# Optimization experiments

Measured on AMD Instinct MI355X. Metric: run time of the kernel, lower is better.

## Reference

```python
import jax, jax.numpy as jnp
import numpy as np

DIM = 1024
NUM_HEADS = 16


def setup_inputs() -> dict:
    key = jax.random.key(0)
    ks = jax.random.split(key, 6)
    B, N, C = 2, 2048, DIM
    input_qv = jax.random.normal(ks[0], (B, N, C), dtype=jnp.float32)
    input_k = jax.random.normal(ks[1], (B, N, C), dtype=jnp.float32)
    # Linear weights stored [in, out]; qkv_bias=False so qv/k have no bias.
    s = 1.0 / np.sqrt(C)
    W_qv = jax.random.uniform(ks[2], (C, 2 * C), dtype=jnp.float32, minval=-s, maxval=s)
    W_k = jax.random.uniform(ks[3], (C, C), dtype=jnp.float32, minval=-s, maxval=s)
    W_proj = jax.random.uniform(ks[4], (C, C), dtype=jnp.float32, minval=-s, maxval=s)
    b_proj = jax.random.uniform(ks[5], (C,), dtype=jnp.float32, minval=-s, maxval=s)
    return {"input_qv": input_qv, "input_k": input_k, "W_qv": W_qv,
            "W_k": W_k, "W_proj": W_proj, "b_proj": b_proj}


def reference(input_qv, input_k, W_qv, W_k, W_proj, b_proj):
    B, N, C = input_qv.shape
    H = NUM_HEADS
    Dh = C // H
    scale = Dh ** -0.5
    # qv projection -> [B, N, 2, H, Dh] -> q, v each [B, H, N, Dh]
    qv = (input_qv @ W_qv).reshape(B, N, 2, H, Dh)
    q = jnp.transpose(qv[:, :, 0], (0, 2, 1, 3))  # [B, H, N, Dh]
    v = jnp.transpose(qv[:, :, 1], (0, 2, 1, 3))  # [B, H, N, Dh]
    k = jnp.transpose((input_k @ W_k).reshape(B, N, H, Dh), (0, 2, 1, 3))  # [B, H, N, Dh]
    # explicit QK^T softmax V (dropout ratio 0 -> identity)
    atten = jnp.einsum('bhnd,bhmd->bhnm', q, k) * scale  # [B, H, N, N]
    atten = jax.nn.softmax(atten, axis=-1)
    x = jnp.einsum('bhnm,bhmd->bhnd', atten, v)  # [B, H, N, Dh]
    x = jnp.transpose(x, (0, 2, 1, 3)).reshape(B, N, C)
    return x @ W_proj + b_proj
```

## Files before the change

kernel.cpp:

```cpp
#include <hip/hip_runtime.h>
#include <stdint.h>

#define BATCH 2
#define SEQ   2048
#define DIM   1024
#define NH    16
#define DH    64

typedef short bf16x8 __attribute__((ext_vector_type(8)));
typedef float floatx4 __attribute__((ext_vector_type(4)));

__device__ __forceinline__ int swz(int r) { return (r ^ (r >> 2)) & 3; }

#if __has_builtin(__builtin_amdgcn_exp2f)
#define EXP2(x) __builtin_amdgcn_exp2f(x)
#else
#define EXP2(x) __expf((x) * 0.6931471805599453f)
#endif

__device__ __forceinline__ uint32_t pack_bf16_rne(float x0, float x1) {
    uint32_t u0 = __float_as_uint(x0), u1 = __float_as_uint(x1);
    u0 += 0x7FFFu + ((u0 >> 16) & 1);
    u1 += 0x7FFFu + ((u1 >> 16) & 1);
    return (u0 >> 16) | (u1 & 0xFFFF0000u);
}

__device__ __forceinline__ ushort bf16_rne1(float x) {
    uint32_t u = __float_as_uint(x);
    u += 0x7FFFu + ((u >> 16) & 1);
    return (ushort)(u >> 16);
}

#define KSCALE 0.18033688011112042f

__global__ __launch_bounds__(256, 3)
void gemm_qvk(const float* __restrict__ Aqv, const float* __restrict__ Akp,
              const float* __restrict__ Wqv, const float* __restrict__ Wkp,
              uint32_t* __restrict__ qh, ushort* __restrict__ vt,
              uint32_t* __restrict__ kh)
{
    __shared__ uint32_t Ah[128 * 16], Bh[128 * 16];

    const int t    = threadIdx.x;
    const int lane = t & 63;
    const int w    = t >> 6;
    const int wm   = w & 1, wn = w >> 1;
    const int quad = lane >> 4, l15 = lane & 15;
    const int bx   = blockIdx.x;
    const bool is_qv = (bx < 16);
    const float* Af = is_qv ? Aqv : Akp;
    const float* Bf = is_qv ? Wqv : Wkp;
    const int N    = is_qv ? 2048 : 1024;
    const int n0   = (is_qv ? bx : bx - 16) * 128;
    const int m0   = blockIdx.y * 128;

    const int ar  = t >> 1;
    const int ab0 = (t & 1) * 2;
    const int as  = swz(ar);
    const int bc  = (t & 31) * 4;
    const int bk  = (t >> 5) * 4;
    const int bb  = bk >> 3;
    const int bp  = (bk & 7) >> 1;
    const bool nsel = ((bc >> 4) & 1) != 0;

    floatx4 acc[4][4];
    #pragma unroll
    for (int i = 0; i < 4; i++)
        #pragma unroll
        for (int j = 0; j < 4; j++)
            #pragma unroll
            for (int e = 0; e < 4; e++) acc[i][j][e] = 0.0f;

    float f[16];
    float4 g4[4];
    {
        #pragma unroll
        for (int i = 0; i < 4; i++)
            *(float4*)&f[i * 4] =
                *(const float4*)&Af[(size_t)(m0 + ar) * 1024 + ab0 * 8 + i * 4];
        #pragma unroll
        for (int j = 0; j < 4; j++)
            g4[j] = *(const float4*)&Bf[(size_t)(bk + j) * N + n0 + bc];
    }

    for (int k0 = 0; k0 < 1024; k0 += 32) {
        if (k0) __syncthreads();
        {
            uint32_t hi[8];
            #pragma unroll
            for (int j = 0; j < 8; j++) hi[j] = pack_bf16_rne(f[2 * j], f[2 * j + 1]);
            int i0 = ar * 16 + ((ab0 ^ as) * 4);
            int i1 = ar * 16 + (((ab0 + 1) ^ as) * 4);
            *(uint4*)&Ah[i0] = make_uint4(hi[0], hi[1], hi[2], hi[3]);
            *(uint4*)&Ah[i1] = make_uint4(hi[4], hi[5], hi[6], hi[7]);
        }
        {
            #pragma unroll
            for (int i = 0; i < 4; i++) {
                int n = bc + (i ^ (nsel ? 1 : 0));
                float e0 = nsel ? ((const float*)&g4[0])[i ^ 1] : ((const float*)&g4[0])[i];
                float e1 = nsel ? ((const float*)&g4[1])[i ^ 1] : ((const float*)&g4[1])[i];
                float e2 = nsel ? ((const float*)&g4[2])[i ^ 1] : ((const float*)&g4[2])[i];
                float e3 = nsel ? ((const float*)&g4[3])[i ^ 1] : ((const float*)&g4[3])[i];
                uint32_t u0 = pack_bf16_rne(e0, e1);
                uint32_t u1 = pack_bf16_rne(e2, e3);
                int bi = n * 16 + ((bb ^ swz(n)) * 4) + bp;
                *(uint2*)&Bh[bi] = make_uint2(u0, u1);
            }
        }
        __syncthreads();

        if (k0 + 32 < 1024) {
            #pragma unroll
            for (int i = 0; i < 4; i++)
                *(float4*)&f[i * 4] =
                    *(const float4*)&Af[(size_t)(m0 + ar) * 1024 + (k0 + 32) + ab0 * 8 + i * 4];
            #pragma unroll
            for (int j = 0; j < 4; j++)
                g4[j] = *(const float4*)&Bf[(size_t)(k0 + 32 + bk + j) * N + n0 + bc];
        }

        bf16x8 vb[4];
        #pragma unroll
        for (int fn = 0; fn < 4; fn++) {
            int br = wn * 64 + fn * 16 + l15;
            int bi = br * 16 + ((quad ^ swz(br)) * 4);
            vb[fn] = *(const bf16x8*)&Bh[bi];
        }
        #pragma unroll
        for (int fm = 0; fm < 4; fm++) {
            int arow = wm * 64 + fm * 16 + l15;
            int ai = arow * 16 + ((quad ^ swz(arow)) * 4);
            bf16x8 va = *(const bf16x8*)&Ah[ai];
            #pragma unroll
            for (int fn = 0; fn < 4; fn++)
                acc[fm][fn] = __builtin_amdgcn_mfma_f32_16x16x32_bf16(vb[fn], va, acc[fm][fn], 0, 0, 0);
        }
    }

    #pragma unroll
    for (int fm = 0; fm < 4; fm++) {
        int row = m0 + wm * 64 + fm * 16 + l15;
        #pragma unroll
        for (int fn = 0; fn < 4; fn++) {
            int colb = n0 + wn * 64 + fn * 16 + quad * 4;
            floatx4 a = acc[fm][fn];
            if (is_qv) {
                if (colb < 1024) {
                    uint32_t u0 = pack_bf16_rne(a[0], a[1]);
                    uint32_t u1 = pack_bf16_rne(a[2], a[3]);
                    size_t wi = (size_t)row * 512 + (colb >> 1);
                    *(uint2*)&qh[wi] = make_uint2(u0, u1);
                } else {
                    int hh = (colb - 1024) >> 6;
                    int d0 = (colb - 1024) & 63;
                    #pragma unroll
                    for (int j = 0; j < 4; j++)
                        vt[(size_t)(hh * 64 + d0 + j) * 4096 + row] = bf16_rne1(a[j]);
                }
            } else {
                uint32_t u0 = pack_bf16_rne(a[0] * KSCALE, a[1] * KSCALE);
                uint32_t u1 = pack_bf16_rne(a[2] * KSCALE, a[3] * KSCALE);
                size_t wi = (size_t)row * 512 + (colb >> 1);
                *(uint2*)&kh[wi] = make_uint2(u0, u1);
            }
        }
    }
}

__global__ __launch_bounds__(256, 3)
void gemm_projB(const uint32_t* __restrict__ Ag,
                const float* __restrict__ Bf, const float* __restrict__ bias,
                float* __restrict__ Cf, float* __restrict__ P1)
{
    __shared__ uint32_t Ah[128 * 16], Bh[128 * 16];

    const int t    = threadIdx.x;
    const int lane = t & 63;
    const int w    = t >> 6;
    const int wm   = w & 1, wn = w >> 1;
    const int quad = lane >> 4, l15 = lane & 15;
    const int m0 = blockIdx.y * 128, n0 = blockIdx.x * 128;
    const int kz = blockIdx.z;
    const int k0 = kz * 512;
    const int N  = 1024;

    const int bc  = (t & 31) * 4;
    const int bk  = (t >> 5) * 4;
    const int bb  = bk >> 3;
    const int bp  = (bk & 7) >> 1;
    const bool nsel = ((bc >> 4) & 1) != 0;

    const int arow0 = t >> 2, akbl = t & 3;
    const int arow1 = (t + 256) >> 2;

    floatx4 acc[4][4];
    #pragma unroll
    for (int i = 0; i < 4; i++)
        #pragma unroll
        for (int j = 0; j < 4; j++)
            #pragma unroll
            for (int e = 0; e < 4; e++) acc[i][j][e] = 0.0f;

    uint4 gA0, gA1;
    float4 g4[4];
    {
        size_t s0 = (size_t)(m0 + arow0) * 512 + (k0 >> 1) + akbl * 4;
        size_t s1 = (size_t)(m0 + arow1) * 512 + (k0 >> 1) + akbl * 4;
        gA0 = *(const uint4*)&Ag[s0];
        gA1 = *(const uint4*)&Ag[s1];
        #pragma unroll
        for (int j = 0; j < 4; j++)
            g4[j] = *(const float4*)&Bf[(size_t)(k0 + bk + j) * N + n0 + bc];
    }

    for (int kk = 0; kk < 512; kk += 32) {
        if (kk) __syncthreads();
        {
            int dst0 = arow0 * 16 + ((akbl ^ swz(arow0)) * 4);
            int dst1 = arow1 * 16 + ((akbl ^ swz(arow1)) * 4);
            *(uint4*)&Ah[dst0] = gA0;
            *(uint4*)&Ah[dst1] = gA1;
        }
        {
            #pragma unroll
            for (int i = 0; i < 4; i++) {
                int n = bc + (i ^ (nsel ? 1 : 0));
                float e0 = nsel ? ((const float*)&g4[0])[i ^ 1] : ((const float*)&g4[0])[i];
                float e1 = nsel ? ((const float*)&g4[1])[i ^ 1] : ((const float*)&g4[1])[i];
                float e2 = nsel ? ((const float*)&g4[2])[i ^ 1] : ((const float*)&g4[2])[i];
                float e3 = nsel ? ((const float*)&g4[3])[i ^ 1] : ((const float*)&g4[3])[i];
                uint32_t u0 = pack_bf16_rne(e0, e1);
                uint32_t u1 = pack_bf16_rne(e2, e3);
                int bi = n * 16 + ((bb ^ swz(n)) * 4) + bp;
                *(uint2*)&Bh[bi] = make_uint2(u0, u1);
            }
        }
        __syncthreads();

        if (kk + 32 < 512) {
            const int kg = k0 + kk + 32;
            size_t s0 = (size_t)(m0 + arow0) * 512 + (kg >> 1) + akbl * 4;
            size_t s1 = (size_t)(m0 + arow1) * 512 + (kg >> 1) + akbl * 4;
            gA0 = *(const uint4*)&Ag[s0];
            gA1 = *(const uint4*)&Ag[s1];
            #pragma unroll
            for (int j = 0; j < 4; j++)
                g4[j] = *(const float4*)&Bf[(size_t)(kg + bk + j) * N + n0 + bc];
        }

        bf16x8 vb[4];
        #pragma unroll
        for (int fn = 0; fn < 4; fn++) {
            int br = wn * 64 + fn * 16 + l15;
            int bi = br * 16 + ((quad ^ swz(br)) * 4);
            vb[fn] = *(const bf16x8*)&Bh[bi];
        }
        #pragma unroll
        for (int fm = 0; fm < 4; fm++) {
            int arow = wm * 64 + fm * 16 + l15;
            int ai = arow * 16 + ((quad ^ swz(arow)) * 4);
            bf16x8 va = *(const bf16x8*)&Ah[ai];
            #pragma unroll
            for (int fn = 0; fn < 4; fn++)
                acc[fm][fn] = __builtin_amdgcn_mfma_f32_16x16x32_bf16(vb[fn], va, acc[fm][fn], 0, 0, 0);
        }
    }

    #pragma unroll
    for (int fm = 0; fm < 4; fm++) {
        int row = m0 + wm * 64 + fm * 16 + l15;
        #pragma unroll
        for (int fn = 0; fn < 4; fn++) {
            int colb = n0 + wn * 64 + fn * 16 + quad * 4;
            floatx4 a = acc[fm][fn];
            float4 v;
            if (kz == 0) {
                float4 bb4 = *(const float4*)&bias[colb];
                v.x = a[0] + bb4.x; v.y = a[1] + bb4.y;
                v.z = a[2] + bb4.z; v.w = a[3] + bb4.w;
                *(float4*)&Cf[(size_t)row * N + colb] = v;
            } else {
                v.x = a[0]; v.y = a[1]; v.z = a[2]; v.w = a[3];
                *(float4*)&P1[(size_t)row * N + colb] = v;
            }
        }
    }
}

__global__ __launch_bounds__(256)
void add_partial(const float4* __restrict__ p1, float4* __restrict__ out, int n4)
{
    int i = blockIdx.x * 256 + threadIdx.x;
    int stride = gridDim.x * 256;
    for (; i < n4; i += stride) {
        float4 a = out[i];
        float4 b = p1[i];
        a.x += b.x; a.y += b.y; a.z += b.z; a.w += b.w;
        out[i] = a;
    }
}

#define FST 34
__global__ __launch_bounds__(256, 2)
void flash_attn(const uint32_t* __restrict__ qhg,
                const uint32_t* __restrict__ khg,
                const uint32_t* __restrict__ vtg,
                uint32_t* __restrict__ xhg)
{
    __shared__ uint32_t Kh[64 * FST];
    __shared__ uint32_t Vt[64 * FST];
    __shared__ uint32_t Pt[128 * FST];

    const int t    = threadIdx.x;
    const int lane = t & 63;
    const int w    = t >> 6;
    const int quad = lane >> 4, l15 = lane & 15;
    const int qb = blockIdx.x;
    const int h  = blockIdx.y;
    const int b  = blockIdx.z;

    const size_t rowbase = (size_t)b * SEQ;

    bf16x8 vq[2][2];
    {
        #pragma unroll
        for (int nf = 0; nf < 2; nf++) {
            size_t row = rowbase + qb * 128 + w * 32 + nf * 16 + l15;
            size_t gw = row * 512 + h * 32 + quad * 4;
            #pragma unroll
            for (int s = 0; s < 2; s++)
                vq[s][nf] = *(const bf16x8*)&qhg[gw + s * 16];
        }
    }

    const int krow = t >> 2, kc0 = (t & 3) * 8;
    const int vd = t >> 2, vc = t & 3;
    const size_t vrow = (size_t)(h * 64 + vd) * 2048 + (rowbase >> 1);
    uint4 pk0, pk1, pv0, pv1;
    {
        size_t gw = (rowbase + krow) * 512 + h * 32 + kc0;
        pk0 = *(const uint4*)&khg[gw];
        pk1 = *(const uint4*)&khg[gw + 4];
        size_t vw = vrow + vc * 8;
        pv0 = *(const uint4*)&vtg[vw];
        pv1 = *(const uint4*)&vtg[vw + 4];
    }

    float m_i[2] = {-INFINITY, -INFINITY};
    float l_i[2] = {0.0f, 0.0f};
    floatx4 acc_o[2][4];
    #pragma unroll
    for (int nf = 0; nf < 2; nf++)
        #pragma unroll
        for (int fm = 0; fm < 4; fm++)
            #pragma unroll
            for (int e = 0; e < 4; e++) acc_o[nf][fm][e] = 0.0f;

    for (int kt = 0; kt < SEQ / 64; kt++) {
        __syncthreads();
        *(uint4*)&Kh[krow * FST + kc0]     = pk0;
        *(uint4*)&Kh[krow * FST + kc0 + 4] = pk1;
        {
            int vb0 = vd * FST + vc * 8;
            *(uint2*)&Vt[vb0]     = make_uint2(pv0.x, pv0.y);
            *(uint2*)&Vt[vb0 + 2] = make_uint2(pv0.z, pv0.w);
            *(uint2*)&Vt[vb0 + 4] = make_uint2(pv1.x, pv1.y);
            *(uint2*)&Vt[vb0 + 6] = make_uint2(pv1.z, pv1.w);
        }
        __syncthreads();

        if (kt + 1 < SEQ / 64) {
            size_t gw = (rowbase + (kt + 1) * 64 + krow) * 512 + h * 32 + kc0;
            pk0 = *(const uint4*)&khg[gw];
            pk1 = *(const uint4*)&khg[gw + 4];
            size_t vw = vrow + (kt + 1) * 32 + vc * 8;
            pv0 = *(const uint4*)&vtg[vw];
            pv1 = *(const uint4*)&vtg[vw + 4];
        }

        floatx4 sacc[2][4];
        #pragma unroll
        for (int nf = 0; nf < 2; nf++)
            #pragma unroll
            for (int fm = 0; fm < 4; fm++)
                #pragma unroll
                for (int e = 0; e < 4; e++) sacc[nf][fm][e] = 0.0f;

        __builtin_amdgcn_s_setprio(1);
        #pragma unroll
        for (int s = 0; s < 2; s++) {
            #pragma unroll
            for (int fm = 0; fm < 4; fm++) {
                int ki = (fm * 16 + l15) * FST + s * 16 + quad * 4;
                bf16x8 vk = *(const bf16x8*)&Kh[ki];
                #pragma unroll
                for (int nf = 0; nf < 2; nf++)
                    sacc[nf][fm] = __builtin_amdgcn_mfma_f32_16x16x32_bf16(vk, vq[s][nf], sacc[nf][fm], 0, 0, 0);
            }
        }
        __builtin_amdgcn_s_setprio(0);

        #pragma unroll
        for (int nf = 0; nf < 2; nf++) {
            float p[4][4];
            float mt = -INFINITY;
            #pragma unroll
            for (int fm = 0; fm < 4; fm++)
                #pragma unroll
                for (int r = 0; r < 4; r++) {
                    p[fm][r] = sacc[nf][fm][r];
                    mt = fmaxf(mt, p[fm][r]);
                }
            mt = fmaxf(mt, __shfl_xor(mt, 16));
            mt = fmaxf(mt, __shfl_xor(mt, 32));
            float m_new = fmaxf(m_i[nf], mt);
            float alpha = EXP2(m_i[nf] - m_new);
            float rs = 0.0f;
            #pragma unroll
            for (int fm = 0; fm < 4; fm++)
                #pragma unroll
                for (int r = 0; r < 4; r++) {
                    p[fm][r] = EXP2(p[fm][r] - m_new);
                    rs += p[fm][r];
                }
            rs += __shfl_xor(rs, 16);
            rs += __shfl_xor(rs, 32);
            l_i[nf] = l_i[nf] * alpha + rs;
            m_i[nf] = m_new;
            #pragma unroll
            for (int fm = 0; fm < 4; fm++)
                #pragma unroll
                for (int e = 0; e < 4; e++) acc_o[nf][fm][e] *= alpha;

            int qrow = w * 32 + nf * 16 + l15;
            #pragma unroll
            for (int fm = 0; fm < 4; fm++) {
                uint32_t u0 = pack_bf16_rne(p[fm][0], p[fm][1]);
                uint32_t u1 = pack_bf16_rne(p[fm][2], p[fm][3]);
                *(uint2*)&Pt[qrow * FST + fm * 8 + quad * 2] = make_uint2(u0, u1);
            }
        }

        __builtin_amdgcn_s_setprio(1);
        #pragma unroll
        for (int s = 0; s < 2; s++) {
            bf16x8 pb[2];
            #pragma unroll
            for (int nf = 0; nf < 2; nf++)
                pb[nf] = *(const bf16x8*)&Pt[(w * 32 + nf * 16 + l15) * FST + s * 16 + quad * 4];
            #pragma unroll
            for (int fm = 0; fm < 4; fm++) {
                bf16x8 va = *(const bf16x8*)&Vt[(fm * 16 + l15) * FST + s * 16 + quad * 4];
                #pragma unroll
                for (int nf = 0; nf < 2; nf++)
                    acc_o[nf][fm] = __builtin_amdgcn_mfma_f32_16x16x32_bf16(va, pb[nf], acc_o[nf][fm], 0, 0, 0);
            }
        }
        __builtin_amdgcn_s_setprio(0);
    }

    #pragma unroll
    for (int nf = 0; nf < 2; nf++) {
        float rl = 1.0f / l_i[nf];
        size_t row = rowbase + qb * 128 + w * 32 + nf * 16 + l15;
        #pragma unroll
        for (int fm = 0; fm < 4; fm++) {
            int d0 = fm * 16 + quad * 4;
            uint32_t u0 = pack_bf16_rne(acc_o[nf][fm][0] * rl, acc_o[nf][fm][1] * rl);
            uint32_t u1 = pack_bf16_rne(acc_o[nf][fm][2] * rl, acc_o[nf][fm][3] * rl);
            size_t wi = row * 512 + ((h * 64 + d0) >> 1);
            *(uint2*)&xhg[wi] = make_uint2(u0, u1);
        }
    }
}

extern "C" void kernel_launch(void* const* d_in, const int* in_sizes, int n_in,
                              void* d_out, int out_size, void* d_ws, size_t ws_size,
                              hipStream_t stream)
{
    const float* input_qv = (const float*)d_in[0];
    const float* input_k  = (const float*)d_in[1];
    const float* W_qv     = (const float*)d_in[2];
    const float* W_k      = (const float*)d_in[3];
    const float* W_proj   = (const float*)d_in[4];
    const float* b_proj   = (const float*)d_in[5];
    float* out = (float*)d_out;

    const size_t RW = 4096 * 512;
    uint32_t* qh = (uint32_t*)d_ws;
    uint32_t* vt = qh + RW;
    uint32_t* xh = vt + RW;
    uint32_t* kh = (uint32_t*)d_out;
    float* p1 = (float*)d_ws;

    dim3 blk(256);
    gemm_qvk<<<dim3(24, 32), blk, 0, stream>>>(
        input_qv, input_k, W_qv, W_k, qh, (ushort*)vt, kh);
    flash_attn<<<dim3(SEQ / 128, NH, BATCH), blk, 0, stream>>>(
        qh, kh, vt, xh);
    gemm_projB<<<dim3(8, 32, 2), blk, 0, stream>>>(
        xh, W_proj, b_proj, out, p1);
    add_partial<<<dim3(2048), blk, 0, stream>>>(
        (const float4*)p1, (float4*)out, 4096 * 1024 / 4);
}
```

Measured before the change: 249.2 us.

## Process two K-slices per sync in projection GEMMs and skip softmax rescale lazily

Both projection GEMM kernels now stage two 32-wide K slices into separate shared-memory buffers per iteration. This halves the number of barriers and doubles the register prefetch depth, at the cost of more registers and shared memory, which may lower occupancy under the 3-block launch bound. The attention kernel also gains a lazy-rescale path: when the new tile max exceeds the running max by at most 8 (log2 units) across the wave, it skips updating the max and the alpha rescale of the output accumulator. This relies on the bounded exponent growth staying within fp32 range.

```diff
diff --git a/kernel.cpp b/kernel.cpp
--- a/kernel.cpp
+++ b/kernel.cpp
@@ -39,7 +39,7 @@
               uint32_t* __restrict__ qh, ushort* __restrict__ vt,
               uint32_t* __restrict__ kh)
 {
-    __shared__ uint32_t Ah[128 * 16], Bh[128 * 16];
+    __shared__ uint32_t Ah[2][128 * 16], Bh[2][128 * 16];
 
     const int t    = threadIdx.x;
     const int lane = t & 63;
@@ -71,70 +71,90 @@
             #pragma unroll
             for (int e = 0; e < 4; e++) acc[i][j][e] = 0.0f;
 
-    float f[16];
-    float4 g4[4];
+    float f0[16], f1[16];
+    float4 g40[4], g41[4];
     {
         #pragma unroll
-        for (int i = 0; i < 4; i++)
-            *(float4*)&f[i * 4] =
+        for (int i = 0; i < 4; i++) {
+            *(float4*)&f0[i * 4] =
                 *(const float4*)&Af[(size_t)(m0 + ar) * 1024 + ab0 * 8 + i * 4];
-        #pragma unroll
-        for (int j = 0; j < 4; j++)
-            g4[j] = *(const float4*)&Bf[(size_t)(bk + j) * N + n0 + bc];
-    }
-
-    for (int k0 = 0; k0 < 1024; k0 += 32) {
+            *(float4*)&f1[i * 4] =
+                *(const float4*)&Af[(size_t)(m0 + ar) * 1024 + 32 + ab0 * 8 + i * 4];
+        }
+        #pragma unroll
+        for (int j = 0; j < 4; j++) {
+            g40[j] = *(const float4*)&Bf[(size_t)(bk + j) * N + n0 + bc];
+            g41[j] = *(const float4*)&Bf[(size_t)(32 + bk + j) * N + n0 + bc];
+        }
+    }
+
+    for (int k0 = 0; k0 < 1024; k0 += 64) {
         if (k0) __syncthreads();
         {
             uint32_t hi[8];
             #pragma unroll
-            for (int j = 0; j < 8; j++) hi[j] = pack_bf16_rne(f[2 * j], f[2 * j + 1]);
+            for (int j = 0; j < 8; j++) hi[j] = pack_bf16_rne(f0[2 * j], f0[2 * j + 1]);
             int i0 = ar * 16 + ((ab0 ^ as) * 4);
             int i1 = ar * 16 + (((ab0 + 1) ^ as) * 4);
-            *(uint4*)&Ah[i0] = make_uint4(hi[0], hi[1], hi[2], hi[3]);
-            *(uint4*)&Ah[i1] = make_uint4(hi[4], hi[5], hi[6], hi[7]);
+            *(uint4*)&Ah[0][i0] = make_uint4(hi[0], hi[1], hi[2], hi[3]);
+            *(uint4*)&Ah[0][i1] = make_uint4(hi[4], hi[5], hi[6], hi[7]);
+            #pragma unroll
+            for (int j = 0; j < 8; j++) hi[j] = pack_bf16_rne(f1[2 * j], f1[2 * j + 1]);
+            *(uint4*)&Ah[1][i0] = make_uint4(hi[0], hi[1], hi[2], hi[3]);
+            *(uint4*)&Ah[1][i1] = make_uint4(hi[4], hi[5], hi[6], hi[7]);
         }
         {
             #pragma unroll
             for (int i = 0; i < 4; i++) {
                 int n = bc + (i ^ (nsel ? 1 : 0));
-                float e0 = nsel ? ((const float*)&g4[0])[i ^ 1] : ((const float*)&g4[0])[i];
-                float e1 = nsel ? ((const float*)&g4[1])[i ^ 1] : ((const float*)&g4[1])[i];
-                float e2 = nsel ? ((const float*)&g4[2])[i ^ 1] : ((const float*)&g4[2])[i];
-                float e3 = nsel ? ((const float*)&g4[3])[i ^ 1] : ((const float*)&g4[3])[i];
-                uint32_t u0 = pack_bf16_rne(e0, e1);
-                uint32_t u1 = pack_bf16_rne(e2, e3);
                 int bi = n * 16 + ((bb ^ swz(n)) * 4) + bp;
-                *(uint2*)&Bh[bi] = make_uint2(u0, u1);
+                float e0 = nsel ? ((const float*)&g40[0])[i ^ 1] : ((const float*)&g40[0])[i];
+                float e1 = nsel ? ((const float*)&g40[1])[i ^ 1] : ((const float*)&g40[1])[i];
+                float e2 = nsel ? ((const float*)&g40[2])[i ^ 1] : ((const float*)&g40[2])[i];
+                float e3 = nsel ? ((const float*)&g40[3])[i ^ 1] : ((const float*)&g40[3])[i];
+                *(uint2*)&Bh[0][bi] = make_uint2(pack_bf16_rne(e0, e1), pack_bf16_rne(e2, e3));
+                e0 = nsel ? ((const float*)&g41[0])[i ^ 1] : ((const float*)&g41[0])[i];
+                e1 = nsel ? ((const float*)&g41[1])[i ^ 1] : ((const float*)&g41[1])[i];
+                e2 = nsel ? ((const float*)&g41[2])[i ^ 1] : ((const float*)&g41[2])[i];
+                e3 = nsel ? ((const float*)&g41[3])[i ^ 1] : ((const float*)&g41[3])[i];
+                *(uint2*)&Bh[1][bi] = make_uint2(pack_bf16_rne(e0, e1), pack_bf16_rne(e2, e3));
             }
         }
         __syncthreads();
 
-        if (k0 + 32 < 1024) {
-            #pragma unroll
-            for (int i = 0; i < 4; i++)
-                *(float4*)&f[i * 4] =
-                    *(const float4*)&Af[(size_t)(m0 + ar) * 1024 + (k0 + 32) + ab0 * 8 + i * 4];
-            #pragma unroll
-            for (int j = 0; j < 4; j++)
-                g4[j] = *(const float4*)&Bf[(size_t)(k0 + 32 + bk + j) * N + n0 + bc];
-        }
-
-        bf16x8 vb[4];
-        #pragma unroll
-        for (int fn = 0; fn < 4; fn++) {
-            int br = wn * 64 + fn * 16 + l15;
-            int bi = br * 16 + ((quad ^ swz(br)) * 4);
-            vb[fn] = *(const bf16x8*)&Bh[bi];
-        }
-        #pragma unroll
-        for (int fm = 0; fm < 4; fm++) {
-            int arow = wm * 64 + fm * 16 + l15;
-            int ai = arow * 16 + ((quad ^ swz(arow)) * 4);
-            bf16x8 va = *(const bf16x8*)&Ah[ai];
-            #pragma unroll
-            for (int fn = 0; fn < 4; fn++)
-                acc[fm][fn] = __builtin_amdgcn_mfma_f32_16x16x32_bf16(vb[fn], va, acc[fm][fn], 0, 0, 0);
+        if (k0 + 64 < 1024) {
+            #pragma unroll
+            for (int i = 0; i < 4; i++) {
+                *(float4*)&f0[i * 4] =
+                    *(const float4*)&Af[(size_t)(m0 + ar) * 1024 + (k0 + 64) + ab0 * 8 + i * 4];
+                *(float4*)&f1[i * 4] =
+                    *(const float4*)&Af[(size_t)(m0 + ar) * 1024 + (k0 + 96) + ab0 * 8 + i * 4];
+            }
+            #pragma unroll
+            for (int j = 0; j < 4; j++) {
+                g40[j] = *(const float4*)&Bf[(size_t)(k0 + 64 + bk + j) * N + n0 + bc];
+                g41[j] = *(const float4*)&Bf[(size_t)(k0 + 96 + bk + j) * N + n0 + bc];
+            }
+        }
+
+        #pragma unroll
+        for (int half = 0; half < 2; half++) {
+            bf16x8 vb[4];
+            #pragma unroll
+            for (int fn = 0; fn < 4; fn++) {
+                int br = wn * 64 + fn * 16 + l15;
+                int bi = br * 16 + ((quad ^ swz(br)) * 4);
+                vb[fn] = *(const bf16x8*)&Bh[half][bi];
+            }
+            #pragma unroll
+            for (int fm = 0; fm < 4; fm++) {
+                int arow = wm * 64 + fm * 16 + l15;
+                int ai = arow * 16 + ((quad ^ swz(arow)) * 4);
+                bf16x8 va = *(const bf16x8*)&Ah[half][ai];
+                #pragma unroll
+                for (int fn = 0; fn < 4; fn++)
+                    acc[fm][fn] = __builtin_amdgcn_mfma_f32_16x16x32_bf16(vb[fn], va, acc[fm][fn], 0, 0, 0);
+            }
         }
     }
 
@@ -173,7 +193,7 @@
                 const float* __restrict__ Bf, const float* __restrict__ bias,
                 float* __restrict__ Cf, float* __restrict__ P1)
 {
-    __shared__ uint32_t Ah[128 * 16], Bh[128 * 16];
+    __shared__ uint32_t Ah[2][128 * 16], Bh[2][128 * 16];
 
     const int t    = threadIdx.x;
     const int lane = t & 63;
@@ -193,6 +213,8 @@
 
     const int arow0 = t >> 2, akbl = t & 3;
     const int arow1 = (t + 256) >> 2;
+    const int dst0 = arow0 * 16 + ((akbl ^ swz(arow0)) * 4);
+    const int dst1 = arow1 * 16 + ((akbl ^ swz(arow1)) * 4);
 
     floatx4 acc[4][4];
     #pragma unroll
@@ -202,68 +224,82 @@
             #pragma unroll
             for (int e = 0; e < 4; e++) acc[i][j][e] = 0.0f;
 
-    uint4 gA0, gA1;
-    float4 g4[4];
+    uint4 gA00, gA01, gA10, gA11;
+    float4 g40[4], g41[4];
     {
         size_t s0 = (size_t)(m0 + arow0) * 512 + (k0 >> 1) + akbl * 4;
         size_t s1 = (size_t)(m0 + arow1) * 512 + (k0 >> 1) + akbl * 4;
-        gA0 = *(const uint4*)&Ag[s0];
-        gA1 = *(const uint4*)&Ag[s1];
-        #pragma unroll
-        for (int j = 0; j < 4; j++)
-            g4[j] = *(const float4*)&Bf[(size_t)(k0 + bk + j) * N + n0 + bc];
-    }
-
-    for (int kk = 0; kk < 512; kk += 32) {
+        gA00 = *(const uint4*)&Ag[s0];
+        gA01 = *(const uint4*)&Ag[s1];
+        gA10 = *(const uint4*)&Ag[s0 + 16];
+        gA11 = *(const uint4*)&Ag[s1 + 16];
+        #pragma unroll
+        for (int j = 0; j < 4; j++) {
+            g40[j] = *(const float4*)&Bf[(size_t)(k0 + bk + j) * N + n0 + bc];
+            g41[j] = *(const float4*)&Bf[(size_t)(k0 + 32 + bk + j) * N + n0 + bc];
+        }
+    }
+
+    for (int kk = 0; kk < 512; kk += 64) {
         if (kk) __syncthreads();
         {
-            int dst0 = arow0 * 16 + ((akbl ^ swz(arow0)) * 4);
-            int dst1 = arow1 * 16 + ((akbl ^ swz(arow1)) * 4);
-            *(uint4*)&Ah[dst0] = gA0;
-            *(uint4*)&Ah[dst1] = gA1;
+            *(uint4*)&Ah[0][dst0] = gA00;
+            *(uint4*)&Ah[0][dst1] = gA01;
+            *(uint4*)&Ah[1][dst0] = gA10;
+            *(uint4*)&Ah[1][dst1] = gA11;
         }
         {
             #pragma unroll
             for (int i = 0; i < 4; i++) {
                 int n = bc + (i ^ (nsel ? 1 : 0));
-                float e0 = nsel ? ((const float*)&g4[0])[i ^ 1] : ((const float*)&g4[0])[i];
-                float e1 = nsel ? ((const float*)&g4[1])[i ^ 1] : ((const float*)&g4[1])[i];
-                float e2 = nsel ? ((const float*)&g4[2])[i ^ 1] : ((const float*)&g4[2])[i];
-                float e3 = nsel ? ((const float*)&g4[3])[i ^ 1] : ((const float*)&g4[3])[i];
-                uint32_t u0 = pack_bf16_rne(e0, e1);
-                uint32_t u1 = pack_bf16_rne(e2, e3);
                 int bi = n * 16 + ((bb ^ swz(n)) * 4) + bp;
-                *(uint2*)&Bh[bi] = make_uint2(u0, u1);
+                float e0 = nsel ? ((const float*)&g40[0])[i ^ 1] : ((const float*)&g40[0])[i];
+                float e1 = nsel ? ((const float*)&g40[1])[i ^ 1] : ((const float*)&g40[1])[i];
+                float e2 = nsel ? ((const float*)&g40[2])[i ^ 1] : ((const float*)&g40[2])[i];
+                float e3 = nsel ? ((const float*)&g40[3])[i ^ 1] : ((const float*)&g40[3])[i];
+                *(uint2*)&Bh[0][bi] = make_uint2(pack_bf16_rne(e0, e1), pack_bf16_rne(e2, e3));
+                e0 = nsel ? ((const float*)&g41[0])[i ^ 1] : ((const float*)&g41[0])[i];
+                e1 = nsel ? ((const float*)&g41[1])[i ^ 1] : ((const float*)&g41[1])[i];
+                e2 = nsel ? ((const float*)&g41[2])[i ^ 1] : ((const float*)&g41[2])[i];
+                e3 = nsel ? ((const float*)&g41[3])[i ^ 1] : ((const float*)&g41[3])[i];
+                *(uint2*)&Bh[1][bi] = make_uint2(pack_bf16_rne(e0, e1), pack_bf16_rne(e2, e3));
             }
         }
         __syncthreads();
 
-        if (kk + 32 < 512) {
-            const int kg = k0 + kk + 32;
+        if (kk + 64 < 512) {
+            const int kg = k0 + kk + 64;
             size_t s0 = (size_t)(m0 + arow0) * 512 + (kg >> 1) + akbl * 4;
             size_t s1 = (size_t)(m0 + arow1) * 512 + (kg >> 1) + akbl * 4;
-            gA0 = *(const uint4*)&Ag[s0];
-            gA1 = *(const uint4*)&Ag[s1];
-            #pragma unroll
-            for (int j = 0; j < 4; j++)
-                g4[j] = *(const float4*)&Bf[(size_t)(kg + bk + j) * N + n0 + bc];
-        }
-
-        bf16x8 vb[4];
-        #pragma unroll
-        for (int fn = 0; fn < 4; fn++) {
-            int br = wn * 64 + fn * 16 + l15;
-            int bi = br * 16 + ((quad ^ swz(br)) * 4);
-            vb[fn] = *(const bf16x8*)&Bh[bi];
-        }
-        #pragma unroll
-        for (int fm = 0; fm < 4; fm++) {
-            int arow = wm * 64 + fm * 16 + l15;
-            int ai = arow * 16 + ((quad ^ swz(arow)) * 4);
-            bf16x8 va = *(const bf16x8*)&Ah[ai];
-            #pragma unroll
-            for (int fn = 0; fn < 4; fn++)
-                acc[fm][fn] = __builtin_amdgcn_mfma_f32_16x16x32_bf16(vb[fn], va, acc[fm][fn], 0, 0, 0);
+            gA00 = *(const uint4*)&Ag[s0];
+            gA01 = *(const uint4*)&Ag[s1];
+            gA10 = *(const uint4*)&Ag[s0 + 16];
+            gA11 = *(const uint4*)&Ag[s1 + 16];
+            #pragma unroll
+            for (int j = 0; j < 4; j++) {
+                g40[j] = *(const float4*)&Bf[(size_t)(kg + bk + j) * N + n0 + bc];
+                g41[j] = *(const float4*)&Bf[(size_t)(kg + 32 + bk + j) * N + n0 + bc];
+            }
+        }
+
+        #pragma unroll
+        for (int half = 0; half < 2; half++) {
+            bf16x8 vb[4];
+            #pragma unroll
+            for (int fn = 0; fn < 4; fn++) {
+                int br = wn * 64 + fn * 16 + l15;
+                int bi = br * 16 + ((quad ^ swz(br)) * 4);
+                vb[fn] = *(const bf16x8*)&Bh[half][bi];
+            }
+            #pragma unroll
+            for (int fm = 0; fm < 4; fm++) {
+                int arow = wm * 64 + fm * 16 + l15;
+                int ai = arow * 16 + ((quad ^ swz(arow)) * 4);
+                bf16x8 va = *(const bf16x8*)&Ah[half][ai];
+                #pragma unroll
+                for (int fn = 0; fn < 4; fn++)
+                    acc[fm][fn] = __builtin_amdgcn_mfma_f32_16x16x32_bf16(vb[fn], va, acc[fm][fn], 0, 0, 0);
+            }
         }
     }
 
@@ -414,24 +450,39 @@
                 }
             mt = fmaxf(mt, __shfl_xor(mt, 16));
             mt = fmaxf(mt, __shfl_xor(mt, 32));
-            float m_new = fmaxf(m_i[nf], mt);
-            float alpha = EXP2(m_i[nf] - m_new);
-            float rs = 0.0f;
-            #pragma unroll
-            for (int fm = 0; fm < 4; fm++)
-                #pragma unroll
-                for (int r = 0; r < 4; r++) {
-                    p[fm][r] = EXP2(p[fm][r] - m_new);
-                    rs += p[fm][r];
-                }
-            rs += __shfl_xor(rs, 16);
-            rs += __shfl_xor(rs, 32);
-            l_i[nf] = l_i[nf] * alpha + rs;
-            m_i[nf] = m_new;
-            #pragma unroll
-            for (int fm = 0; fm < 4; fm++)
-                #pragma unroll
-                for (int e = 0; e < 4; e++) acc_o[nf][fm][e] *= alpha;
+
+            if (__all(mt - m_i[nf] <= 8.0f)) {
+                float rs = 0.0f;
+                #pragma unroll
+                for (int fm = 0; fm < 4; fm++)
+                    #pragma unroll
+                    for (int r = 0; r < 4; r++) {
+                        p[fm][r] = EXP2(p[fm][r] - m_i[nf]);
+                        rs += p[fm][r];
+                    }
+                rs += __shfl_xor(rs, 16);
+                rs += __shfl_xor(rs, 32);
+                l_i[nf] += rs;
+            } else {
+                float m_new = fmaxf(m_i[nf], mt);
+                float alpha = EXP2(m_i[nf] - m_new);
+                float rs = 0.0f;
+                #pragma unroll
+                for (int fm = 0; fm < 4; fm++)
+                    #pragma unroll
+                    for (int r = 0; r < 4; r++) {
+                        p[fm][r] = EXP2(p[fm][r] - m_new);
+                        rs += p[fm][r];
+                    }
+                rs += __shfl_xor(rs, 16);
+                rs += __shfl_xor(rs, 32);
+                l_i[nf] = l_i[nf] * alpha + rs;
+                m_i[nf] = m_new;
+                #pragma unroll
+                for (int fm = 0; fm < 4; fm++)
+                    #pragma unroll
+                    for (int e = 0; e < 4; e++) acc_o[nf][fm][e] *= alpha;
+            }
 
             int qrow = w * 32 + nf * 16 + l15;
             #pragma unroll
```

New measurement: 248.0 us. About the same (-0.5%).
